# Kernel tuning notes

Hardware: AMD Instinct MI355X
Metric: run time of the kernel (lower is better)

The kernel has to match this reference:

```python
import jax, jax.numpy as jnp
import numpy as np

T, B, E, H, V, L = 128, 64, 1024, 1024, 10000, 2


def setup_inputs() -> dict:
    key = jax.random.key(0)
    ks = jax.random.split(key, 10)
    k = 1.0 / np.sqrt(H)
    u = lambda kk, shape, a: jax.random.uniform(kk, shape, jnp.float32, -a, a)
    return {
        "emb_table": u(ks[0], (V, E), 0.1),
        "W_in0": u(ks[1], (H, E), k),   # first layer input weight (no bias in linear_W)
        "Wh0": u(ks[2], (H, H), k),
        "b0": u(ks[3], (H,), k),
        "W_in1": u(ks[4], (H, H), k),
        "Wh1": u(ks[5], (H, H), k),
        "b1": u(ks[6], (H,), k),
        "Wdec": u(ks[7], (V, H), 0.1),
        "bdec": jnp.zeros((V,), jnp.float32),
        "hidden": jnp.zeros((L, B, H), jnp.float32),
        "tokens": jax.random.randint(ks[8], (T, B), 0, V, jnp.int32),
    }


def reference(emb_table, W_in0, Wh0, b0, W_in1, Wh1, b1, Wdec, bdec, hidden, tokens):
    # dp_keep_prob = 1.0 -> dropout is identity
    x_emb = emb_table[tokens]  # [T, B, E]

    def step(h, x):
        # h: [L, B, H]; x: [B, E]
        h0 = jnp.tanh(x @ W_in0.T + h[0] @ Wh0.T + b0)
        h1 = jnp.tanh(h0 @ W_in1.T + h[1] @ Wh1.T + b1)
        logits_t = h1 @ Wdec.T + bdec  # [B, V]
        return jnp.stack([h0, h1]), logits_t

    h_final, logits = jax.lax.scan(step, hidden, x_emb)
    return logits, h_final  # [T, B, V], [L, B, H]
```

## Files before the change

### kernel.cpp

```cpp
#include <hip/hip_runtime.h>
#include <hip/hip_bf16.h>
#include <stdint.h>

typedef __bf16 bf16_t;
typedef __bf16 bf16x8 __attribute__((ext_vector_type(8)));
typedef __bf16 bf16x4 __attribute__((ext_vector_type(4)));
typedef float  floatx4 __attribute__((ext_vector_type(4)));

#define T_STEPS 128
#define BATCH   64
#define EDIM    1024
#define HDIM    1024
#define VOCAB   10000
#define MROWS   (T_STEPS * BATCH)
#define RNN_BLOCKS 128
#define BH      (BATCH * HDIM)
#define FSTRIDE 16

__device__ __forceinline__ floatx4 mfma16(bf16x8 a, bf16x8 b, floatx4 c) {
    return __builtin_amdgcn_mfma_f32_16x16x32_bf16(a, b, c, 0, 0, 0);
}

__device__ __forceinline__ void gl_lds16(const bf16_t* g, bf16_t* l) {
    __builtin_amdgcn_global_load_lds(
        (const __attribute__((address_space(1))) void*)g,
        (__attribute__((address_space(3))) void*)l, 16, 0, 0);
}

__device__ __forceinline__ void store_bf16_bypass(bf16_t* p, float v) {
    union { bf16_t b; unsigned short u; } cv;
    cv.b = (bf16_t)v;
    unsigned int d = cv.u;
    asm volatile("global_store_short %0, %1, off sc0 sc1"
                 :: "v"(p), "v"(d) : "memory");
}


__global__ void f2b_kernel(const float* __restrict__ s, bf16_t* __restrict__ d, int n) {
    int i = (blockIdx.x * blockDim.x + threadIdx.x) * 4;
    if (i < n) {
        float4 v = *(const float4*)(s + i);
        bf16x4 o;
        o.x = (bf16_t)v.x; o.y = (bf16_t)v.y; o.z = (bf16_t)v.z; o.w = (bf16_t)v.w;
        *(bf16x4*)(d + i) = o;
    }
}

__global__ void gather_kernel(const float* __restrict__ emb, const int* __restrict__ tok,
                              bf16_t* __restrict__ X) {
    int row = blockIdx.x;
    int t = tok[row];
    int e = threadIdx.x * 4;
    float4 v = *(const float4*)(emb + (size_t)t * EDIM + e);
    bf16x4 o;
    o.x = (bf16_t)v.x; o.y = (bf16_t)v.y; o.z = (bf16_t)v.z; o.w = (bf16_t)v.w;
    *(bf16x4*)(X + (size_t)row * EDIM + e) = o;
}

__global__ void init_state_kernel(const float* __restrict__ hidden,
                                  bf16_t* __restrict__ h0all, bf16_t* __restrict__ h1all,
                                  int* __restrict__ flags) {
    int i = blockIdx.x * blockDim.x + threadIdx.x;
    h0all[i] = (bf16_t)hidden[i];
    h1all[i] = (bf16_t)hidden[BATCH * HDIM + i];
    if (i < 128 * FSTRIDE) flags[i] = 0;
}


template <int OUT_BF16>
__global__ __launch_bounds__(256) void gemm_kernel(
    const bf16_t* __restrict__ A, const bf16_t* __restrict__ W,
    const float* __restrict__ bias, void* __restrict__ out,
    int M, int N, int K)
{
    const int tid  = threadIdx.x;
    const int lane = tid & 63;
    const int wave = tid >> 6;
    const int wm   = wave & 1;
    const int wn   = wave >> 1;
    const int quad = lane >> 4;
    const int l16  = lane & 15;
    const int mTile = blockIdx.y * 128;
    const int nTile = blockIdx.x * 128;

    __shared__ __align__(16) bf16_t sA[128 * 32];
    __shared__ __align__(16) bf16_t sW[128 * 32];

    const floatx4 fzero = {0.f, 0.f, 0.f, 0.f};
    floatx4 acc[4][4];
    #pragma unroll
    for (int i = 0; i < 4; ++i)
        #pragma unroll
        for (int j = 0; j < 4; ++j) acc[i][j] = fzero;

    for (int kk = 0; kk < K; kk += 32) {
        __syncthreads();
        #pragma unroll
        for (int j = 0; j < 2; ++j) {
            int c   = tid + j * 256;
            int row = c >> 2;
            int sub = c & 3;
            gl_lds16(A + (size_t)(mTile + row) * K + kk + sub * 8, sA + c * 8);
            int wrow = nTile + row;
            if (wrow >= N) wrow = N - 1;
            gl_lds16(W + (size_t)wrow * K + kk + sub * 8, sW + c * 8);
        }
        __syncthreads();
        bf16x8 af[4], wf[4];
        #pragma unroll
        for (int mi = 0; mi < 4; ++mi)
            af[mi] = *(const bf16x8*)(sA + (wm * 64 + mi * 16 + l16) * 32 + quad * 8);
        #pragma unroll
        for (int ni = 0; ni < 4; ++ni)
            wf[ni] = *(const bf16x8*)(sW + (wn * 64 + ni * 16 + l16) * 32 + quad * 8);
        #pragma unroll
        for (int mi = 0; mi < 4; ++mi)
            #pragma unroll
            for (int ni = 0; ni < 4; ++ni)
                acc[mi][ni] = mfma16(af[mi], wf[ni], acc[mi][ni]);
    }

    #pragma unroll
    for (int ni = 0; ni < 4; ++ni) {
        int col = nTile + wn * 64 + ni * 16 + l16;
        if (col < N) {
            float bv = bias[col];
            #pragma unroll
            for (int mi = 0; mi < 4; ++mi) {
                #pragma unroll
                for (int r = 0; r < 4; ++r) {
                    int row = mTile + wm * 64 + mi * 16 + quad * 4 + r;
                    float v = acc[mi][ni][r] + bv;
                    if (OUT_BF16) ((bf16_t*)out)[(size_t)row * N + col] = (bf16_t)v;
                    else          ((float*)out)[(size_t)row * N + col] = v;
                }
            }
        }
    }
}


__global__ __launch_bounds__(256, 1) void rnn_step_kernel(
    const bf16_t* __restrict__ X0,
    const bf16_t* __restrict__ Wh0b,
    const bf16_t* __restrict__ Win1b,
    const bf16_t* __restrict__ Wh1b,
    const float*  __restrict__ b1,
    bf16_t* __restrict__ h0all,
    bf16_t* __restrict__ h1all,
    int* __restrict__ flags)
{
    __shared__ __align__(16) char smem[65536];
    const int tid  = threadIdx.x;
    const int lane = tid & 63;
    const int wave = tid >> 6;
    const int quad = lane >> 4;
    const int l16  = lane & 15;
    const bool isL1 = blockIdx.x >= 64;
    const int cb    = blockIdx.x & 63;
    const int cbase = cb * 16;
    const int colg  = cbase + l16;
    const int arow  = (wave * 16 + l16) * HDIM;
    const int orow0 = wave * 16 + quad * 4;
    const floatx4 fzero = {0.f, 0.f, 0.f, 0.f};
    int* f0 = flags;
    int* f1 = flags + 64 * FSTRIDE;

    {
        const bf16_t* W0 = isL1 ? Win1b : Wh0b;
        for (int c = tid; c < 2048; c += 256) {
            int kc2 = c >> 6, ln = c & 63;
            const bf16_t* src = W0 + (size_t)(cbase + (ln & 15)) * HDIM + kc2 * 32 + (ln >> 4) * 8;
            *(int4*)(smem + c * 16) = *(const int4*)src;
        }
        if (isL1) {
            for (int c = tid; c < 2048; c += 256) {
                int kc2 = c >> 6, ln = c & 63;
                const bf16_t* src = Wh1b + (size_t)(cbase + (ln & 15)) * HDIM + kc2 * 32 + (ln >> 4) * 8;
                *(int4*)(smem + 32768 + c * 16) = *(const int4*)src;
            }
        }
    }
    __syncthreads();

    if (!isL1) {
        float xr[4];
        #pragma unroll
        for (int r = 0; r < 4; ++r)
            xr[r] = (float)X0[(size_t)(orow0 + r) * HDIM + colg];
        int vc = 0;
        for (int t = 0; t < T_STEPS; ++t) {
            if (t > 0) {
                if (wave == 0) {
                    while (!__all(vc >= t)) {
                        if (vc < t) {
                            vc = __hip_atomic_load(&f0[lane * FSTRIDE], __ATOMIC_RELAXED,
                                                   __HIP_MEMORY_SCOPE_AGENT);
                            if (vc < t) __builtin_amdgcn_s_sleep(1);
                        }
                    }
                }
                __syncthreads();
            }
            const bf16_t* Ap = h0all + (size_t)t * BH;
            bf16x8 av[32];
            #pragma unroll
            for (int kc = 0; kc < 32; ++kc)
                av[kc] = *(const bf16x8*)(Ap + arow + kc * 32 + quad * 8);
            float xn[4];
            if (t + 1 < T_STEPS) {
                #pragma unroll
                for (int r = 0; r < 4; ++r)
                    xn[r] = (float)X0[((size_t)(t + 1) * BATCH + orow0 + r) * HDIM + colg];
            }
            __builtin_amdgcn_sched_barrier(0);
            floatx4 a0 = fzero, a1 = fzero;
            #pragma unroll
            for (int kc = 0; kc < 32; ++kc) {
                bf16x8 wv = *(const bf16x8*)(smem + kc * 1024 + lane * 16);
                if (kc & 1) a1 = mfma16(av[kc], wv, a1);
                else        a0 = mfma16(av[kc], wv, a0);
            }
            bf16_t* dst = h0all + (size_t)(t + 1) * BH;
            #pragma unroll
            for (int r = 0; r < 4; ++r)
                store_bf16_bypass(dst + (size_t)(orow0 + r) * HDIM + colg,
                                  tanhf(xr[r] + a0[r] + a1[r]));
            if (t + 1 < T_STEPS) {
                #pragma unroll
                for (int r = 0; r < 4; ++r) xr[r] = xn[r];
            }
            asm volatile("s_waitcnt vmcnt(0)" ::: "memory");
            __syncthreads();
            if (tid == 0)
                __hip_atomic_store(&f0[cb * FSTRIDE], t + 1, __ATOMIC_RELAXED,
                                   __HIP_MEMORY_SCOPE_AGENT);
        }
    } else {
        const float bb = b1[colg];
        int vc0 = 0, vc1 = 0;
        for (int t = 0; t < T_STEPS; ++t) {
            if (wave == 0) {
                while (!__all(vc0 >= t + 1)) {
                    if (vc0 < t + 1) {
                        vc0 = __hip_atomic_load(&f0[lane * FSTRIDE], __ATOMIC_RELAXED,
                                                __HIP_MEMORY_SCOPE_AGENT);
                        if (vc0 < t + 1) __builtin_amdgcn_s_sleep(1);
                    }
                }
            }
            __syncthreads();
            const bf16_t* A0 = h0all + (size_t)(t + 1) * BH;
            bf16x8 av0[32];
            #pragma unroll
            for (int kc = 0; kc < 32; ++kc)
                av0[kc] = *(const bf16x8*)(A0 + arow + kc * 32 + quad * 8);
            __builtin_amdgcn_sched_barrier(0);
            floatx4 aA = fzero, aB = fzero;
            #pragma unroll
            for (int kc = 0; kc < 32; ++kc) {
                bf16x8 wv1 = *(const bf16x8*)(smem + kc * 1024 + lane * 16);
                if (kc & 1) aB = mfma16(av0[kc], wv1, aB);
                else        aA = mfma16(av0[kc], wv1, aA);
            }
            if (t > 0) {
                if (wave == 0) {
                    while (!__all(vc1 >= t)) {
                        if (vc1 < t) {
                            vc1 = __hip_atomic_load(&f1[lane * FSTRIDE], __ATOMIC_RELAXED,
                                                    __HIP_MEMORY_SCOPE_AGENT);
                            if (vc1 < t) __builtin_amdgcn_s_sleep(1);
                        }
                    }
                }
                __syncthreads();
            }
            const bf16_t* A1 = h1all + (size_t)t * BH;
            bf16x8 av1[32];
            #pragma unroll
            for (int kc = 0; kc < 32; ++kc)
                av1[kc] = *(const bf16x8*)(A1 + arow + kc * 32 + quad * 8);
            __builtin_amdgcn_sched_barrier(0);
            #pragma unroll
            for (int kc = 0; kc < 32; ++kc) {
                bf16x8 wv2 = *(const bf16x8*)(smem + 32768 + kc * 1024 + lane * 16);
                if (kc & 1) aB = mfma16(av1[kc], wv2, aB);
                else        aA = mfma16(av1[kc], wv2, aA);
            }
            bf16_t* dst = h1all + (size_t)(t + 1) * BH;
            #pragma unroll
            for (int r = 0; r < 4; ++r)
                store_bf16_bypass(dst + (size_t)(orow0 + r) * HDIM + colg,
                                  tanhf(aA[r] + aB[r] + bb));
            asm volatile("s_waitcnt vmcnt(0)" ::: "memory");
            __syncthreads();
            if (tid == 0)
                __hip_atomic_store(&f1[cb * FSTRIDE], t + 1, __ATOMIC_RELAXED,
                                   __HIP_MEMORY_SCOPE_AGENT);
        }
    }
}

__global__ void finalize_kernel(const bf16_t* __restrict__ h0all,
                                const bf16_t* __restrict__ h1all,
                                float* __restrict__ out) {
    int i = blockIdx.x * blockDim.x + threadIdx.x;
    const size_t OUT0 = (size_t)MROWS * VOCAB;
    out[OUT0 + i]                = (float)h0all[(size_t)T_STEPS * BATCH * HDIM + i];
    out[OUT0 + BATCH * HDIM + i] = (float)h1all[(size_t)T_STEPS * BATCH * HDIM + i];
}


extern "C" void kernel_launch(void* const* d_in, const int* in_sizes, int n_in,
                              void* d_out, int out_size, void* d_ws, size_t ws_size,
                              hipStream_t stream) {
    (void)in_sizes; (void)n_in; (void)out_size; (void)ws_size;
    const float* emb    = (const float*)d_in[0];
    const float* W_in0  = (const float*)d_in[1];
    const float* Wh0    = (const float*)d_in[2];
    const float* b0     = (const float*)d_in[3];
    const float* W_in1  = (const float*)d_in[4];
    const float* Wh1    = (const float*)d_in[5];
    const float* b1     = (const float*)d_in[6];
    const float* Wdec   = (const float*)d_in[7];
    const float* bdec   = (const float*)d_in[8];
    const float* hidden = (const float*)d_in[9];
    const int*   tokens = (const int*)d_in[10];
    float* out = (float*)d_out;

    char* ws = (char*)d_ws;
    auto alloc = [&](size_t bytes) {
        char* p = ws; ws += (bytes + 255) & ~(size_t)255; return p;
    };
    bf16_t* Xemb  = (bf16_t*)alloc((size_t)MROWS * EDIM * 2);
    bf16_t* X0    = (bf16_t*)alloc((size_t)MROWS * HDIM * 2);
    bf16_t* Win0b = (bf16_t*)alloc((size_t)HDIM * EDIM * 2);
    bf16_t* Wh0b  = (bf16_t*)alloc((size_t)HDIM * HDIM * 2);
    bf16_t* Win1b = (bf16_t*)alloc((size_t)HDIM * HDIM * 2);
    bf16_t* Wh1b  = (bf16_t*)alloc((size_t)HDIM * HDIM * 2);
    bf16_t* Wdecb = (bf16_t*)alloc((size_t)VOCAB * HDIM * 2);
    bf16_t* h1all = (bf16_t*)alloc((size_t)(T_STEPS + 1) * BATCH * HDIM * 2);
    bf16_t* h0all = (bf16_t*)alloc((size_t)(T_STEPS + 1) * BATCH * HDIM * 2);
    int*    flags = (int*)alloc(128 * FSTRIDE * 4);

    f2b_kernel<<<dim3(HDIM * EDIM / 1024), 256, 0, stream>>>(W_in0, Win0b, HDIM * EDIM);
    f2b_kernel<<<dim3(HDIM * HDIM / 1024), 256, 0, stream>>>(Wh0,   Wh0b,  HDIM * HDIM);
    f2b_kernel<<<dim3(HDIM * HDIM / 1024), 256, 0, stream>>>(W_in1, Win1b, HDIM * HDIM);
    f2b_kernel<<<dim3(HDIM * HDIM / 1024), 256, 0, stream>>>(Wh1,   Wh1b,  HDIM * HDIM);
    f2b_kernel<<<dim3(VOCAB * HDIM / 1024), 256, 0, stream>>>(Wdec, Wdecb, VOCAB * HDIM);
    gather_kernel<<<dim3(MROWS), 256, 0, stream>>>(emb, tokens, Xemb);
    init_state_kernel<<<dim3(256), 256, 0, stream>>>(hidden, h0all, h1all, flags);

    gemm_kernel<1><<<dim3(HDIM / 128, MROWS / 128), 256, 0, stream>>>(
        Xemb, Win0b, b0, X0, MROWS, HDIM, EDIM);

    rnn_step_kernel<<<dim3(RNN_BLOCKS), 256, 0, stream>>>(
        X0, Wh0b, Win1b, Wh1b, b1, h0all, h1all, flags);

    gemm_kernel<0><<<dim3((VOCAB + 127) / 128, MROWS / 128), 256, 0, stream>>>(
        h1all + BATCH * HDIM, Wdecb, bdec, out, MROWS, VOCAB, HDIM);

    finalize_kernel<<<dim3(256), 256, 0, stream>>>(h0all, h1all, out);
}
```

Before: 1.742 ms.

## Overlap decoder GEMM with recurrent steps inside persistent RNN kernel

```diff
diff --git a/kernel.cpp b/kernel.cpp
--- a/kernel.cpp
+++ b/kernel.cpp
@@ -14,8 +14,11 @@
 #define VOCAB   10000
 #define MROWS   (T_STEPS * BATCH)
 #define RNN_BLOCKS 128
+#define DEC_BLOCKS 128
 #define BH      (BATCH * HDIM)
 #define FSTRIDE 16
+#define VTILES  79
+#define NUNITS  (64 * VTILES)
 
 __device__ __forceinline__ floatx4 mfma16(bf16x8 a, bf16x8 b, floatx4 c) {
     return __builtin_amdgcn_mfma_f32_16x16x32_bf16(a, b, c, 0, 0, 0);
@@ -146,6 +149,9 @@
     const bf16_t* __restrict__ Win1b,
     const bf16_t* __restrict__ Wh1b,
     const float*  __restrict__ b1,
+    const bf16_t* __restrict__ Wdecb,
+    const float*  __restrict__ bdec,
+    float* __restrict__ logits,
     bf16_t* __restrict__ h0all,
     bf16_t* __restrict__ h1all,
     int* __restrict__ flags)
@@ -156,15 +162,91 @@
     const int wave = tid >> 6;
     const int quad = lane >> 4;
     const int l16  = lane & 15;
+    int* f0 = flags;
+    int* f1 = flags + 64 * FSTRIDE;
+    const floatx4 fzero = {0.f, 0.f, 0.f, 0.f};
+
+    if (blockIdx.x >= RNN_BLOCKS) {
+        const int d  = blockIdx.x - RNN_BLOCKS;
+        const int wm = wave & 1;
+        const int wn = wave >> 1;
+        bf16_t* sA = (bf16_t*)smem;
+        bf16_t* sW = (bf16_t*)(smem + 8192);
+        const bf16_t* Adec = h1all + BH;
+        int vc = 0;
+        for (int u = d; u < NUNITS; u += DEC_BLOCKS) {
+            const int tp = u / VTILES;
+            const int vt = u - tp * VTILES;
+            const int need = 2 * tp + 2;
+            if (wave == 0) {
+                while (!__all(vc >= need)) {
+                    if (vc < need) {
+                        vc = __hip_atomic_load(&f1[lane * FSTRIDE], __ATOMIC_RELAXED,
+                                               __HIP_MEMORY_SCOPE_AGENT);
+                        if (vc < need) __builtin_amdgcn_s_sleep(32);
+                    }
+                }
+            }
+            __syncthreads();
+            const int mTile = tp * 128;
+            const int nTile = vt * 128;
+            floatx4 acc[4][4];
+            #pragma unroll
+            for (int i = 0; i < 4; ++i)
+                #pragma unroll
+                for (int j = 0; j < 4; ++j) acc[i][j] = fzero;
+            for (int kk = 0; kk < HDIM; kk += 32) {
+                __syncthreads();
+                #pragma unroll
+                for (int j = 0; j < 2; ++j) {
+                    int c   = tid + j * 256;
+                    int row = c >> 2;
+                    int sub = c & 3;
+                    gl_lds16(Adec + (size_t)(mTile + row) * HDIM + kk + sub * 8, sA + c * 8);
+                    int wrow = nTile + row;
+                    if (wrow >= VOCAB) wrow = VOCAB - 1;
+                    gl_lds16(Wdecb + (size_t)wrow * HDIM + kk + sub * 8, sW + c * 8);
+                }
+                __syncthreads();
+                bf16x8 af[4], wf[4];
+                #pragma unroll
+                for (int mi = 0; mi < 4; ++mi)
+                    af[mi] = *(const bf16x8*)(sA + (wm * 64 + mi * 16 + l16) * 32 + quad * 8);
+                #pragma unroll
+                for (int ni = 0; ni < 4; ++ni)
+                    wf[ni] = *(const bf16x8*)(sW + (wn * 64 + ni * 16 + l16) * 32 + quad * 8);
+                #pragma unroll
+                for (int mi = 0; mi < 4; ++mi)
+                    #pragma unroll
+                    for (int ni = 0; ni < 4; ++ni)
+                        acc[mi][ni] = mfma16(af[mi], wf[ni], acc[mi][ni]);
+            }
+            #pragma unroll
+            for (int ni = 0; ni < 4; ++ni) {
+                int col = nTile + wn * 64 + ni * 16 + l16;
+                if (col < VOCAB) {
+                    float bv = bdec[col];
+                    #pragma unroll
+                    for (int mi = 0; mi < 4; ++mi) {
+                        #pragma unroll
+                        for (int r = 0; r < 4; ++r) {
+                            int row = mTile + wm * 64 + mi * 16 + quad * 4 + r;
+                            logits[(size_t)row * VOCAB + col] = acc[mi][ni][r] + bv;
+                        }
+                    }
+                }
+            }
+            __syncthreads();
+        }
+        return;
+    }
+
     const bool isL1 = blockIdx.x >= 64;
     const int cb    = blockIdx.x & 63;
     const int cbase = cb * 16;
     const int colg  = cbase + l16;
     const int arow  = (wave * 16 + l16) * HDIM;
     const int orow0 = wave * 16 + quad * 4;
-    const floatx4 fzero = {0.f, 0.f, 0.f, 0.f};
-    int* f0 = flags;
-    int* f1 = flags + 64 * FSTRIDE;
 
     {
         const bf16_t* W0 = isL1 ? Win1b : Wh0b;
@@ -354,11 +436,8 @@
     gemm_kernel<1><<<dim3(HDIM / 128, MROWS / 128), 256, 0, stream>>>(
         Xemb, Win0b, b0, X0, MROWS, HDIM, EDIM);
 
-    rnn_step_kernel<<<dim3(RNN_BLOCKS), 256, 0, stream>>>(
-        X0, Wh0b, Win1b, Wh1b, b1, h0all, h1all, flags);
-
-    gemm_kernel<0><<<dim3((VOCAB + 127) / 128, MROWS / 128), 256, 0, stream>>>(
-        h1all + BATCH * HDIM, Wdecb, bdec, out, MROWS, VOCAB, HDIM);
+    rnn_step_kernel<<<dim3(RNN_BLOCKS + DEC_BLOCKS), 256, 0, stream>>>(
+        X0, Wh0b, Win1b, Wh1b, b1, Wdecb, bdec, out, h0all, h1all, flags);
 
     finalize_kernel<<<dim3(256), 256, 0, stream>>>(h0all, h1all, out);
 }
```

Result: faster. 1.489 ms (-14.5%).
